# Kernel optimization log

Hardware: AMD Instinct MI355X
Metric: run time of the kernel (lower is better)

Reference implementation:

```python
import jax, jax.numpy as jnp
import numpy as np

DIM = 1024
HEADS = 8
EV = DIM  # dim*expand - dim with expand=2
P = 2.0   # power-softmax exponent
EPS = 1e-5


def setup_inputs() -> dict:
    key = jax.random.key(0)
    k1, k2, k3 = jax.random.split(key, 3)
    B, L = 4, 2048
    x = jax.random.normal(k1, (B, L, DIM), dtype=jnp.float32)
    gamma = jnp.ones((DIM,), dtype=jnp.float32)
    beta = jnp.zeros((DIM,), dtype=jnp.float32)
    # torch nn.Linear weights are [out_features, in_features]
    w_qkv = jax.random.normal(k2, (5 * DIM, DIM), dtype=jnp.float32) * (DIM ** -0.5)
    w_out = jax.random.normal(k3, (DIM, 2 * DIM), dtype=jnp.float32) * ((2 * DIM) ** -0.5)
    return {"x": x, "gamma": gamma, "beta": beta, "w_qkv": w_qkv, "w_out": w_out}


def _layernorm(x, gamma, beta):
    xf = x.astype(jnp.float32)
    mu = jnp.mean(xf, axis=-1, keepdims=True)
    var = jnp.mean(jnp.square(xf - mu), axis=-1, keepdims=True)
    return ((xf - mu) * jax.lax.rsqrt(var + EPS)) * gamma + beta


def _p_softmax(scores, scale, p):
    # scores: [B,H,L,L] with -inf on masked entries
    s = scores.astype(jnp.float32) * scale
    if p == 1.0:
        return jax.nn.softmax(s, axis=-1)
    lse = jax.nn.logsumexp(s * p, axis=-1, keepdims=True) / p
    return jnp.exp(s - lse)


def _attention(q, k, v, heads, p):
    B, L, D = q.shape
    hd = D // heads
    q = q.reshape(B, L, heads, hd).transpose(0, 2, 1, 3)  # bhld
    k = k.reshape(B, L, heads, hd).transpose(0, 2, 1, 3)
    v = v.reshape(B, L, heads, hd).transpose(0, 2, 1, 3)
    scores = jnp.einsum('bhqd,bhkd->bhqk', q, k)
    mask = jnp.tril(jnp.ones((L, L), dtype=bool))
    scores = jnp.where(mask, scores, -jnp.inf)
    probs = _p_softmax(scores, hd ** -0.5, p).astype(q.dtype)
    out = jnp.einsum('bhqk,bhkd->bhqd', probs, v)
    return out.transpose(0, 2, 1, 3).reshape(B, L, D)


def reference(x, gamma, beta, w_qkv, w_out):
    h = _layernorm(x, gamma, beta).astype(x.dtype)
    proj = h @ w_qkv.T  # [B,L,5*DIM]
    q, k, v, lin, pre = jnp.split(proj, np.cumsum([DIM, DIM, DIM, EV]), axis=-1)
    attn = _attention(q, k, v, HEADS, P)
    branch = jnp.concatenate([lin * jax.nn.gelu(pre, approximate=False), attn], axis=-1)
    return x + branch @ w_out.T
```

## Files before the change

kernel.cpp:

```cpp
#include <hip/hip_runtime.h>
#include <hip/hip_bf16.h>
#include <math.h>

#define DIMD 1024
#define LSEQ 2048
#define BATCH 4
#define NHEAD 8
#define HD 128
#define NROWS (BATCH*LSEQ)
#define PROJC (5*DIMD)
#define BRC (2*DIMD)

typedef __attribute__((ext_vector_type(8))) short short8;
typedef __attribute__((ext_vector_type(4))) short short4v;
typedef __attribute__((ext_vector_type(4))) float floatx4;

__device__ __forceinline__ float bf2f(short s) {
  unsigned int u = ((unsigned int)(unsigned short)s) << 16;
  return __builtin_bit_cast(float, u);
}
__device__ __forceinline__ short f2bf(float f) {
  unsigned int u = __builtin_bit_cast(unsigned int, f);
  unsigned int lsb = (u >> 16) & 1u;
  u += 0x7fffu + lsb;
  return (short)(u >> 16);
}

__device__ __forceinline__ void gl2lds16(const short* g, short* l) {
  __builtin_amdgcn_global_load_lds(
      (const __attribute__((address_space(1))) unsigned int*)(unsigned long long)g,
      (__attribute__((address_space(3))) unsigned int*)(unsigned int)(unsigned long long)l,
      16, 0, 0);
}

__global__ __launch_bounds__(256) void cvt_kernel(const float* __restrict__ src,
    short* __restrict__ dst, int n4) {
  int i = blockIdx.x * 256 + threadIdx.x;
  if (i >= n4) return;
  float4 v = *(const float4*)(src + (size_t)i * 4);
  short4v o;
  o[0] = f2bf(v.x); o[1] = f2bf(v.y); o[2] = f2bf(v.z); o[3] = f2bf(v.w);
  *(short4v*)(dst + (size_t)i * 4) = o;
}

__global__ __launch_bounds__(256) void ln_kernel(const float* __restrict__ x,
    const float* __restrict__ gamma, const float* __restrict__ beta,
    short* __restrict__ h) {
  int row = blockIdx.x;
  int c = threadIdx.x * 4;
  const float* xr = x + (size_t)row * DIMD;
  float4 v = *(const float4*)(xr + c);
  float f[4] = {v.x, v.y, v.z, v.w};
  float sum = 0.f, sq = 0.f;
  for (int i = 0; i < 4; ++i) { sum += f[i]; sq += f[i]*f[i]; }
  for (int off = 1; off < 64; off <<= 1) {
    sum += __shfl_xor(sum, off);
    sq  += __shfl_xor(sq, off);
  }
  __shared__ float red[8];
  int wid = threadIdx.x >> 6;
  if ((threadIdx.x & 63) == 0) { red[wid*2] = sum; red[wid*2+1] = sq; }
  __syncthreads();
  sum = red[0]+red[2]+red[4]+red[6];
  sq  = red[1]+red[3]+red[5]+red[7];
  float mu = sum * (1.0f/DIMD);
  float var = sq * (1.0f/DIMD) - mu*mu;
  float rstd = rsqrtf(var + 1e-5f);
  float4 g = *(const float4*)(gamma + c);
  float4 bb = *(const float4*)(beta + c);
  float gg[4] = {g.x, g.y, g.z, g.w};
  float bv[4] = {bb.x, bb.y, bb.z, bb.w};
  short4v o;
  for (int i = 0; i < 4; ++i)
    o[i] = f2bf((f[i] - mu) * rstd * gg[i] + bv[i]);
  *(short4v*)(h + (size_t)row * DIMD + c) = o;
}

template<int MODE>
__global__ __launch_bounds__(256) void gemm_bt(const short* __restrict__ A,
    const short* __restrict__ W, const float* __restrict__ X,
    void* __restrict__ Cv, int M, int N, int K) {
  __shared__ __align__(16) short As[128*64];
  __shared__ __align__(16) short Ws[128*64];
  int tid = threadIdx.x;
  int row0 = blockIdx.y * 128;
  int col0 = blockIdx.x * 128;
  int lane = tid & 63, wv = tid >> 6;
  int wr = (wv >> 1) * 64, wc = (wv & 1) * 64;
  int quad = lane >> 4, l16 = lane & 15;
  floatx4 acc[4][4] = {};
  int srow = lane >> 3;
  int gq = ((lane & 7) - srow) & 7;
  const short* Ag = A + (size_t)(row0 + wv*8 + srow) * K + gq*8;
  const short* Wg = W + (size_t)(col0 + wv*8 + srow) * K + gq*8;
  short* Al = As + wv*8*64;
  short* Wl = Ws + wv*8*64;
  int qsr0 = (((quad)     + (l16 & 7)) & 7) * 8;
  int qsr1 = (((quad + 4) + (l16 & 7)) & 7) * 8;
  for (int k0 = 0; k0 < K; k0 += 64) {
    __syncthreads();
    for (int c = 0; c < 4; ++c) {
      gl2lds16(Ag + k0 + (size_t)(c*32)*K, Al + c*32*64);
      gl2lds16(Wg + k0 + (size_t)(c*32)*K, Wl + c*32*64);
    }
    __syncthreads();
    short8 af[4], wf[4];
    for (int i = 0; i < 4; ++i) af[i] = *(const short8*)&As[(wr + i*16 + l16)*64 + qsr0];
    for (int j = 0; j < 4; ++j) wf[j] = *(const short8*)&Ws[(wc + j*16 + l16)*64 + qsr0];
    for (int i = 0; i < 4; ++i)
      for (int j = 0; j < 4; ++j)
        acc[i][j] = __builtin_amdgcn_mfma_f32_16x16x32_bf16(af[i], wf[j], acc[i][j], 0, 0, 0);
    for (int i = 0; i < 4; ++i) af[i] = *(const short8*)&As[(wr + i*16 + l16)*64 + qsr1];
    for (int j = 0; j < 4; ++j) wf[j] = *(const short8*)&Ws[(wc + j*16 + l16)*64 + qsr1];
    for (int i = 0; i < 4; ++i)
      for (int j = 0; j < 4; ++j)
        acc[i][j] = __builtin_amdgcn_mfma_f32_16x16x32_bf16(af[i], wf[j], acc[i][j], 0, 0, 0);
  }
  for (int i = 0; i < 4; ++i) {
    int r0 = row0 + wr + i*16 + quad*4;
    for (int j = 0; j < 4; ++j) {
      int cc = col0 + wc + j*16 + l16;
      for (int r = 0; r < 4; ++r) {
        float v = acc[i][j][r];
        size_t idx = (size_t)(r0 + r) * N + cc;
        if (MODE == 0) {
          ((short*)Cv)[idx] = f2bf(v);
        } else {
          ((float*)Cv)[idx] = v + X[idx];
        }
      }
    }
  }
}

__global__ __launch_bounds__(256) void gelu_kernel(const short* __restrict__ proj,
    short* __restrict__ branch) {
  int row = blockIdx.x;
  int c = threadIdx.x * 4;
  const short* pr = proj + (size_t)row * PROJC;
  short4v lin = *(const short4v*)(pr + 3*DIMD + c);
  short4v pre = *(const short4v*)(pr + 4*DIMD + c);
  short4v o;
  for (int i = 0; i < 4; ++i) {
    float xx = bf2f(pre[i]);
    float g = 0.5f * xx * (1.f + erff(xx * 0.70710678118654752f));
    o[i] = f2bf(bf2f(lin[i]) * g);
  }
  *(short4v*)(branch + (size_t)row * BRC + c) = o;
}

__global__ __launch_bounds__(256) void vt_kernel(const short* __restrict__ proj,
    short* __restrict__ vt) {
  int bh = blockIdx.y;
  int b = bh >> 3, hh = bh & 7;
  int l0 = blockIdx.x * 64;
  __shared__ short Ls[64][136];
  int tid = threadIdx.x;
  int r = tid >> 4, c = (tid & 15) * 8;
  const short* Vp = proj + (size_t)b * LSEQ * PROJC + 2*DIMD + hh*HD;
  for (int p = 0; p < 4; ++p)
    *(short8*)&Ls[r + p*16][c] = *(const short8*)(Vp + (size_t)(l0 + r + p*16) * PROJC + c);
  __syncthreads();
  int d = tid >> 1, lh = (tid & 1) * 32;
  short* outp = vt + ((size_t)bh * HD + d) * LSEQ + l0 + lh;
  for (int g = 0; g < 4; ++g) {
    short8 o;
    for (int j = 0; j < 8; ++j) o[j] = Ls[lh + g*8 + j][d];
    *(short8*)(outp + g*8) = o;
  }
}

__global__ __launch_bounds__(512) void attn_kernel(const short* __restrict__ proj,
    const short* __restrict__ vt, short* __restrict__ branch) {
  int bh = blockIdx.y;
  int b = bh >> 3, hh = bh & 7;
  int bid = blockIdx.x;
  int tid = threadIdx.x;
  int wv = tid >> 6, lane = tid & 63, quad = lane >> 4, l16 = lane & 15;
  int qsel = (wv < 4) ? bid : (31 - bid);
  int qw = qsel * 64 + (wv & 3) * 16;

  const short* Qp  = proj + (size_t)b * LSEQ * PROJC + hh*HD;
  const short* Kp  = Qp + DIMD;
  const short* VTp = vt + (size_t)bh * HD * LSEQ;

  __shared__ short Ks[64][136];
  __shared__ short Vs[128][76];
  __shared__ short Ps[8][16][44];

  short8 qf[4];
  {
    const short* qrow = Qp + (size_t)(qw + l16) * PROJC;
    for (int s = 0; s < 4; ++s) qf[s] = *(const short8*)(qrow + s*32 + quad*8);
  }
  float lsum[4] = {0.f, 0.f, 0.f, 0.f};
  floatx4 O[8] = {};

  const float scale = 0.08838834764831845f;
  int NT = 32 - bid;
  int krow = tid >> 4;
  int kcol = (tid & 15) * 8;
  int vd = tid >> 2;
  int vk = (tid & 3) * 8;
  for (int kt = 0; kt < NT; ++kt) {
    int kb64 = kt * 64;
    short8 kv0 = *(const short8*)(Kp + (size_t)(kb64 + krow) * PROJC + kcol);
    short8 kv1 = *(const short8*)(Kp + (size_t)(kb64 + 32 + krow) * PROJC + kcol);
    short8 vv0 = *(const short8*)(VTp + (size_t)vd * LSEQ + kb64 + vk);
    short8 vv1 = *(const short8*)(VTp + (size_t)vd * LSEQ + kb64 + 32 + vk);
    __syncthreads();
    *(short8*)&Ks[krow][kcol]      = kv0;
    *(short8*)&Ks[krow + 32][kcol] = kv1;
    *(short8*)&Vs[vd][vk]          = vv0;
    *(short8*)&Vs[vd][32 + vk]     = vv1;
    __syncthreads();
    for (int hf = 0; hf < 2; ++hf) {
      int kb = kb64 + hf*32;
      if (kb <= qw + 15) {
        floatx4 s0 = {0.f,0.f,0.f,0.f}, s1 = {0.f,0.f,0.f,0.f};
        for (int s = 0; s < 4; ++s) {
          short8 kf0 = *(const short8*)&Ks[hf*32 + l16][s*32 + quad*8];
          short8 kf1 = *(const short8*)&Ks[hf*32 + 16 + l16][s*32 + quad*8];
          s0 = __builtin_amdgcn_mfma_f32_16x16x32_bf16(qf[s], kf0, s0, 0, 0, 0);
          s1 = __builtin_amdgcn_mfma_f32_16x16x32_bf16(qf[s], kf1, s1, 0, 0, 0);
        }
        int c0 = kb + l16, c1 = kb + 16 + l16;
        for (int r = 0; r < 4; ++r) {
          int q = qw + quad*4 + r;
          float w0 = (c0 <= q) ? __expf(s0[r] * scale) : 0.f;
          float w1 = (c1 <= q) ? __expf(s1[r] * scale) : 0.f;
          lsum[r] += w0*w0 + w1*w1;
          Ps[wv][quad*4+r][l16]      = f2bf(w0);
          Ps[wv][quad*4+r][16 + l16] = f2bf(w1);
        }
        asm volatile("s_waitcnt lgkmcnt(0)" ::: "memory");
        short8 pf = *(const short8*)&Ps[wv][l16][quad*8];
        for (int t8 = 0; t8 < 8; ++t8) {
          short8 vf = *(const short8*)&Vs[t8*16 + l16][hf*32 + quad*8];
          O[t8] = __builtin_amdgcn_mfma_f32_16x16x32_bf16(pf, vf, O[t8], 0, 0, 0);
        }
      }
    }
    __syncthreads();
  }
  for (int r = 0; r < 4; ++r) {
    float l = lsum[r];
    for (int off = 1; off < 16; off <<= 1) l += __shfl_xor(l, off);
    float inv = rsqrtf(l);
    int q = qw + quad*4 + r;
    short* orow = branch + ((size_t)(b*LSEQ + q)) * BRC + DIMD + hh*HD;
    for (int t8 = 0; t8 < 8; ++t8)
      orow[t8*16 + l16] = f2bf(O[t8][r] * inv);
  }
}

extern "C" void kernel_launch(void* const* d_in, const int* in_sizes, int n_in,
                              void* d_out, int out_size, void* d_ws, size_t ws_size,
                              hipStream_t stream) {
  const float* x     = (const float*)d_in[0];
  const float* gamma = (const float*)d_in[1];
  const float* beta  = (const float*)d_in[2];
  const float* w_qkv = (const float*)d_in[3];
  const float* w_out = (const float*)d_in[4];
  float* out = (float*)d_out;

  char* ws = (char*)d_ws;
  short* h      = (short*)ws;
  short* proj   = (short*)(ws + (size_t)16*1024*1024);
  short* branch = (short*)(ws + (size_t)96*1024*1024);
  short* wq     = (short*)(ws + (size_t)128*1024*1024);
  short* wo     = (short*)(ws + (size_t)138*1024*1024);
  short* vt     = h;

  cvt_kernel<<<(PROJC*DIMD/4 + 255)/256, 256, 0, stream>>>(w_qkv, wq, PROJC*DIMD/4);
  cvt_kernel<<<(DIMD*BRC/4 + 255)/256, 256, 0, stream>>>(w_out, wo, DIMD*BRC/4);
  ln_kernel<<<NROWS, 256, 0, stream>>>(x, gamma, beta, h);
  gemm_bt<0><<<dim3(PROJC/128, NROWS/128), 256, 0, stream>>>(h, wq, nullptr, proj,
                                                             NROWS, PROJC, DIMD);
  gelu_kernel<<<NROWS, 256, 0, stream>>>(proj, branch);
  vt_kernel<<<dim3(LSEQ/64, BATCH*NHEAD), 256, 0, stream>>>(proj, vt);
  attn_kernel<<<dim3(16, BATCH*NHEAD), 512, 0, stream>>>(proj, vt, branch);
  gemm_bt<1><<<dim3(DIMD/128, NROWS/128), 256, 0, stream>>>(branch, wo, x, out,
                                                            NROWS, DIMD, BRC);
}
```

Measured before the change: 363.3 us.

## Prefetch K/V tiles into registers and reorder causal query tiles heaviest-first

```diff
diff --git a/kernel.cpp b/kernel.cpp
--- a/kernel.cpp
+++ b/kernel.cpp
@@ -174,19 +174,19 @@
     const short* __restrict__ vt, short* __restrict__ branch) {
   int bh = blockIdx.y;
   int b = bh >> 3, hh = bh & 7;
-  int bid = blockIdx.x;
+  int bid = 15 - blockIdx.x;
   int tid = threadIdx.x;
   int wv = tid >> 6, lane = tid & 63, quad = lane >> 4, l16 = lane & 15;
-  int qsel = (wv < 4) ? bid : (31 - bid);
+  int qsel = 2*bid + ((wv < 4) ? 0 : 1);
   int qw = qsel * 64 + (wv & 3) * 16;
 
   const short* Qp  = proj + (size_t)b * LSEQ * PROJC + hh*HD;
   const short* Kp  = Qp + DIMD;
   const short* VTp = vt + (size_t)bh * HD * LSEQ;
 
-  __shared__ short Ks[64][136];
-  __shared__ short Vs[128][76];
-  __shared__ short Ps[8][16][44];
+  __shared__ short Ks[64][132];
+  __shared__ short Vs[128][68];
+  __shared__ short Ps[8][16][68];
 
   short8 qf[4];
   {
@@ -197,51 +197,63 @@
   floatx4 O[8] = {};
 
   const float scale = 0.08838834764831845f;
-  int NT = 32 - bid;
+  int NT = 2*bid + 2;
   int krow = tid >> 4;
   int kcol = (tid & 15) * 8;
   int vd = tid >> 2;
   int vk = (tid & 3) * 8;
+  short8 pk0 = *(const short8*)(Kp + (size_t)krow * PROJC + kcol);
+  short8 pk1 = *(const short8*)(Kp + (size_t)(32 + krow) * PROJC + kcol);
+  short8 pv0 = *(const short8*)(VTp + (size_t)vd * LSEQ + vk);
+  short8 pv1 = *(const short8*)(VTp + (size_t)vd * LSEQ + 32 + vk);
   for (int kt = 0; kt < NT; ++kt) {
     int kb64 = kt * 64;
-    short8 kv0 = *(const short8*)(Kp + (size_t)(kb64 + krow) * PROJC + kcol);
-    short8 kv1 = *(const short8*)(Kp + (size_t)(kb64 + 32 + krow) * PROJC + kcol);
-    short8 vv0 = *(const short8*)(VTp + (size_t)vd * LSEQ + kb64 + vk);
-    short8 vv1 = *(const short8*)(VTp + (size_t)vd * LSEQ + kb64 + 32 + vk);
-    __syncthreads();
-    *(short8*)&Ks[krow][kcol]      = kv0;
-    *(short8*)&Ks[krow + 32][kcol] = kv1;
-    *(short8*)&Vs[vd][vk]          = vv0;
-    *(short8*)&Vs[vd][32 + vk]     = vv1;
-    __syncthreads();
-    for (int hf = 0; hf < 2; ++hf) {
-      int kb = kb64 + hf*32;
-      if (kb <= qw + 15) {
-        floatx4 s0 = {0.f,0.f,0.f,0.f}, s1 = {0.f,0.f,0.f,0.f};
-        for (int s = 0; s < 4; ++s) {
-          short8 kf0 = *(const short8*)&Ks[hf*32 + l16][s*32 + quad*8];
-          short8 kf1 = *(const short8*)&Ks[hf*32 + 16 + l16][s*32 + quad*8];
-          s0 = __builtin_amdgcn_mfma_f32_16x16x32_bf16(qf[s], kf0, s0, 0, 0, 0);
-          s1 = __builtin_amdgcn_mfma_f32_16x16x32_bf16(qf[s], kf1, s1, 0, 0, 0);
-        }
-        int c0 = kb + l16, c1 = kb + 16 + l16;
+    __syncthreads();
+    *(short8*)&Ks[krow][kcol]      = pk0;
+    *(short8*)&Ks[krow + 32][kcol] = pk1;
+    *(short8*)&Vs[vd][vk]          = pv0;
+    *(short8*)&Vs[vd][32 + vk]     = pv1;
+    __syncthreads();
+    if (kt + 1 < NT) {
+      int nb = kb64 + 64;
+      pk0 = *(const short8*)(Kp + (size_t)(nb + krow) * PROJC + kcol);
+      pk1 = *(const short8*)(Kp + (size_t)(nb + 32 + krow) * PROJC + kcol);
+      pv0 = *(const short8*)(VTp + (size_t)vd * LSEQ + nb + vk);
+      pv1 = *(const short8*)(VTp + (size_t)vd * LSEQ + nb + 32 + vk);
+    }
+    if (kb64 <= qw + 15) {
+      floatx4 s[4] = {};
+      for (int s4 = 0; s4 < 4; ++s4) {
+        if (kb64 + s4*16 <= qw + 15) {
+          for (int kk = 0; kk < 4; ++kk) {
+            short8 kf = *(const short8*)&Ks[s4*16 + l16][kk*32 + quad*8];
+            s[s4] = __builtin_amdgcn_mfma_f32_16x16x32_bf16(qf[kk], kf, s[s4], 0, 0, 0);
+          }
+        }
+      }
+      for (int s4 = 0; s4 < 4; ++s4) {
+        int cc = kb64 + s4*16 + l16;
         for (int r = 0; r < 4; ++r) {
           int q = qw + quad*4 + r;
-          float w0 = (c0 <= q) ? __expf(s0[r] * scale) : 0.f;
-          float w1 = (c1 <= q) ? __expf(s1[r] * scale) : 0.f;
-          lsum[r] += w0*w0 + w1*w1;
-          Ps[wv][quad*4+r][l16]      = f2bf(w0);
-          Ps[wv][quad*4+r][16 + l16] = f2bf(w1);
-        }
-        asm volatile("s_waitcnt lgkmcnt(0)" ::: "memory");
-        short8 pf = *(const short8*)&Ps[wv][l16][quad*8];
+          float w = (cc <= q) ? __expf(s[s4][r] * scale) : 0.f;
+          lsum[r] += w*w;
+          Ps[wv][quad*4+r][s4*16 + l16] = f2bf(w);
+        }
+      }
+      asm volatile("s_waitcnt lgkmcnt(0)" ::: "memory");
+      short8 pf0 = *(const short8*)&Ps[wv][l16][quad*8];
+      for (int t8 = 0; t8 < 8; ++t8) {
+        short8 vf = *(const short8*)&Vs[t8*16 + l16][quad*8];
+        O[t8] = __builtin_amdgcn_mfma_f32_16x16x32_bf16(pf0, vf, O[t8], 0, 0, 0);
+      }
+      if (kb64 + 32 <= qw + 15) {
+        short8 pf1 = *(const short8*)&Ps[wv][l16][32 + quad*8];
         for (int t8 = 0; t8 < 8; ++t8) {
-          short8 vf = *(const short8*)&Vs[t8*16 + l16][hf*32 + quad*8];
-          O[t8] = __builtin_amdgcn_mfma_f32_16x16x32_bf16(pf, vf, O[t8], 0, 0, 0);
-        }
-      }
-    }
-    __syncthreads();
+          short8 vf = *(const short8*)&Vs[t8*16 + l16][32 + quad*8];
+          O[t8] = __builtin_amdgcn_mfma_f32_16x16x32_bf16(pf1, vf, O[t8], 0, 0, 0);
+        }
+      }
+    }
   }
   for (int r = 0; r < 4; ++r) {
     float l = lsum[r];
```

New measurement: 420.3 us. 15.7% more time.
